# Kernel tuning notes

Hardware: AMD Instinct MI355X
Metric: run time of the kernel (lower is better)

The kernel has to match this reference:

```python
import jax, jax.numpy as jnp
import numpy as np

COORD_W, EDGE_W, COUNT_W, REG_W, CONTRA_W = 1.0, 2.0, 0.1, 0.001, 0.1
MARGIN = 1.0


def setup_inputs() -> dict:
    key = jax.random.key(0)
    ks = jax.random.split(key, 6)
    B, N, D, C = 16, 1024, 128, 2
    return {
        "predicted_coords": jax.random.normal(ks[0], (B, N, C), jnp.float32),
        "points": jax.random.normal(ks[1], (B, N, C), jnp.float32),
        "adjacency_logits": jax.random.normal(ks[2], (B, N, N), jnp.float32),
        "adjacency": jax.random.bernoulli(ks[3], 0.1, (B, N, N)).astype(jnp.float32),
        "node_masks": jnp.ones((B, N), jnp.float32),  # all nodes valid -> n_actual = N
        "predicted_count": jax.random.normal(ks[4], (B, 1), jnp.float32),
        "node_features": jax.random.normal(ks[5], (B, N, D), jnp.float32),
    }


def _bce_with_logits(logits, targets):
    # mean-reduced, numerically stable (matches F.binary_cross_entropy_with_logits)
    return jnp.mean(jnp.maximum(logits, 0.0) - logits * targets
                    + jnp.log1p(jnp.exp(-jnp.abs(logits))))


def _smooth_l1(pred, target):
    d = jnp.abs(pred - target)
    return jnp.mean(jnp.where(d < 1.0, 0.5 * d * d, d - 0.5))


def _contrastive_sample(features, adj):
    # features: [N, D], adj: [N, N]. torch.cdist pairwise euclidean via gram trick.
    nrm = jnp.sum(features * features, axis=-1)              # [N]
    sq = jnp.maximum(nrm[:, None] + nrm[None, :]
                     - 2.0 * (features @ features.T), 0.0)   # [N, N] squared dists
    n = features.shape[0]
    eye = jnp.eye(n, dtype=bool)
    pos_mask = adj > 0.5
    neg_mask = (adj <= 0.5) & (~eye)
    # positive term: mean of distances**2 over positive pairs == mean squared dist
    pos = jnp.sum(jnp.where(pos_mask, sq, 0.0)) / jnp.maximum(jnp.sum(pos_mask), 1)
    dist = jnp.sqrt(jnp.maximum(sq, 1e-12))
    hinge = jnp.square(jax.nn.relu(MARGIN - dist))
    neg = jnp.sum(jnp.where(neg_mask, hinge, 0.0)) / jnp.maximum(jnp.sum(neg_mask), 1)
    return pos + neg


def reference(predicted_coords, points, adjacency_logits, adjacency,
              node_masks, predicted_count, node_features):
    # node_masks are all ones, so the per-sample [:n_actual] slicing is the
    # full tensor; per-sample MSE/BCE means averaged over batch equal global means.
    coord_loss = jnp.mean(jnp.square(predicted_coords - points))
    edge_loss = _bce_with_logits(adjacency_logits, adjacency)
    actual_counts = jnp.sum(node_masks, axis=1)              # [B]
    count_loss = _smooth_l1(predicted_count[:, 0], actual_counts)
    reg_loss = jnp.mean(jnp.square(node_features))
    # contrastive path uses targets['adjacency'] (no predicted_adjacency key)
    contra_loss = jnp.mean(jax.vmap(_contrastive_sample)(node_features, adjacency))
    total = (COORD_W * coord_loss + EDGE_W * edge_loss + COUNT_W * count_loss
             + REG_W * reg_loss + CONTRA_W * contra_loss)
    return total, coord_loss, edge_loss, count_loss, reg_loss, contra_loss
```

## Files before the change

### kernel.cpp

```cpp
#include <hip/hip_runtime.h>
#include <hip/hip_bf16.h>

#define NN    1024
#define DD    128
#define TILE  128
#define PITCH 136
#define SQP   132

typedef __bf16 bf16_t;
typedef bf16_t bf16x8 __attribute__((ext_vector_type(8)));
typedef float  f32x4  __attribute__((ext_vector_type(4)));


__global__ __launch_bounds__(256) void small_losses(
    const float* __restrict__ pcoord, const float* __restrict__ pts,
    const float* __restrict__ masks,  const float* __restrict__ pcount,
    float* __restrict__ ws) {
  __shared__ float sh[4][2];
  float coord = 0.f, cnt = 0.f;

  const int gt = blockIdx.x * 256 + threadIdx.x;
  const int stride = 16 * 256;

  const float4* a4 = (const float4*)pcoord;
  const float4* b4 = (const float4*)pts;
  for (int i = gt; i < 8192; i += stride) {
    float4 a = a4[i], b = b4[i];
    float dx = a.x-b.x, dy = a.y-b.y, dz = a.z-b.z, dw = a.w-b.w;
    coord += dx*dx + dy*dy + dz*dz + dw*dw;
  }
  const float* m = masks + blockIdx.x * NN;
  for (int i = threadIdx.x; i < NN; i += 256) cnt += m[i];

  const int lane = threadIdx.x & 63, w = threadIdx.x >> 6;
  #pragma unroll
  for (int o = 32; o; o >>= 1) {
    coord += __shfl_xor(coord, o);
    cnt   += __shfl_xor(cnt, o);
  }
  if (lane == 0) { sh[w][0] = coord; sh[w][1] = cnt; }
  __syncthreads();
  if (threadIdx.x == 0) {
    float c = 0.f, n = 0.f;
    for (int i = 0; i < 4; ++i) { c += sh[i][0]; n += sh[i][1]; }
    atomicAdd(&ws[0], c);
    float d = fabsf(pcount[blockIdx.x] - n);
    float term = (d < 1.f) ? 0.5f * d * d : d - 0.5f;
    atomicAdd(&ws[2], term);
  }
}

__device__ __forceinline__ void loss_elem(float l, float a, float s, int grow, int gcol,
    float& bsum, float& poss, float& posc, float& negs, float& negc) {
  bsum += fmaxf(l, 0.f) - l * a + log1pf(__expf(-fabsf(l)));
  if (a > 0.5f) {
    poss += s; posc += 1.f;
  } else if (grow != gcol) {
    negc += 1.f;
    if (s < 1.f) {
      float d = sqrtf(fmaxf(s, 1e-12f));
      float h = 1.f - d;
      negs += h * h;
    }
  }
}

__global__ __launch_bounds__(256, 2) void fused_gram_bce(
    const float* __restrict__ logits, const float* __restrict__ adj,
    const float* __restrict__ feat, float* __restrict__ ws) {
  __shared__ __align__(16) char smem[2 * TILE * PITCH * sizeof(bf16_t)];
  bf16_t* lsA = (bf16_t*)smem;
  bf16_t* lsB = (bf16_t*)(smem + TILE * PITCH * sizeof(bf16_t));
  float*  sqb = (float*)smem;
  __shared__ float nrmA[TILE];
  __shared__ float nrmB[TILE];
  __shared__ float red[4][6];

  const int bx  = blockIdx.x;
  const int b   = bx >> 6;
  const int tid = bx & 63;
  const int ti  = (tid >> 3) << 7;
  const int tj  = (tid & 7)  << 7;
  const bool diag = (ti == tj);

  const int t = threadIdx.x;
  const float* fb = feat + (size_t)b * NN * DD;

  float regsum = 0.f;
  #pragma unroll
  for (int it = 0; it < 16; ++it) {
    int cid  = it * 256 + t;
    int tile = cid >> 11;
    int sub  = cid & 2047;
    int row  = sub >> 4;
    int c8   = sub & 15;
    const float* src = fb + (size_t)((tile ? tj : ti) + row) * DD + c8 * 8;
    float4 u = *(const float4*)src;
    float4 v = *(const float4*)(src + 4);
    if (diag && tile == 0)
      regsum += u.x*u.x + u.y*u.y + u.z*u.z + u.w*u.w
              + v.x*v.x + v.y*v.y + v.z*v.z + v.w*v.w;
    bf16_t* dst = (tile ? lsB : lsA) + row * PITCH + c8 * 8;
    dst[0] = (bf16_t)u.x; dst[1] = (bf16_t)u.y; dst[2] = (bf16_t)u.z; dst[3] = (bf16_t)u.w;
    dst[4] = (bf16_t)v.x; dst[5] = (bf16_t)v.y; dst[6] = (bf16_t)v.z; dst[7] = (bf16_t)v.w;
  }
  __syncthreads();

  {
    int row = t & 127;
    const bf16_t* src = (t < 128 ? lsA : lsB) + row * PITCH;
    float s = 0.f;
    #pragma unroll
    for (int c = 0; c < 16; ++c) {
      bf16x8 ch = *(const bf16x8*)(src + c * 8);
      #pragma unroll
      for (int i = 0; i < 8; ++i) { float v = (float)ch[i]; s += v * v; }
    }
    if (t < 128) nrmA[row] = s; else nrmB[row] = s;
  }
  __syncthreads();

  const int lane = t & 63;
  const int wave = t >> 6;
  const int lrow = lane & 15;
  const int quad = lane >> 4;

  f32x4 acc[2][8];
  #pragma unroll
  for (int fr = 0; fr < 2; ++fr)
    #pragma unroll
    for (int fc = 0; fc < 8; ++fc)
      acc[fr][fc] = (f32x4){0.f, 0.f, 0.f, 0.f};

  #pragma unroll
  for (int k0 = 0; k0 < DD; k0 += 32) {
    const int kc = k0 + quad * 8;
    bf16x8 aF0 = *(const bf16x8*)&lsA[(wave * 32 + 0  + lrow) * PITCH + kc];
    bf16x8 aF1 = *(const bf16x8*)&lsA[(wave * 32 + 16 + lrow) * PITCH + kc];
    bf16x8 bF[8];
    #pragma unroll
    for (int fc = 0; fc < 8; ++fc)
      bF[fc] = *(const bf16x8*)&lsB[(fc * 16 + lrow) * PITCH + kc];
    #pragma unroll
    for (int fc = 0; fc < 8; ++fc) {
      acc[0][fc] = __builtin_amdgcn_mfma_f32_16x16x32_bf16(aF0, bF[fc], acc[0][fc], 0, 0, 0);
      acc[1][fc] = __builtin_amdgcn_mfma_f32_16x16x32_bf16(aF1, bF[fc], acc[1][fc], 0, 0, 0);
    }
  }
  __syncthreads();

  #pragma unroll
  for (int fr = 0; fr < 2; ++fr) {
    const int rbase = wave * 32 + fr * 16 + quad * 4;
    #pragma unroll
    for (int fc = 0; fc < 8; ++fc) {
      const int ctile = fc * 16 + lrow;
      const float ncol = nrmB[ctile];
      #pragma unroll
      for (int r = 0; r < 4; ++r) {
        const int rtile = rbase + r;
        sqb[rtile * SQP + ctile] = fmaxf(nrmA[rtile] + ncol - 2.f * acc[fr][fc][r], 0.f);
      }
    }
  }
  __syncthreads();

  float bsum = 0.f, poss = 0.f, posc = 0.f, negs = 0.f, negc = 0.f;
  const size_t base = (size_t)b * NN * NN;
  #pragma unroll
  for (int it = 0; it < 16; ++it) {
    int cid = it * 256 + t;
    int row = cid >> 5;
    int c4  = cid & 31;
    const int grow = ti + row;
    const int gc0  = tj + c4 * 4;
    const size_t gidx = base + (size_t)grow * NN + gc0;
    float4 l = *(const float4*)(logits + gidx);
    float4 a = *(const float4*)(adj + gidx);
    float4 s = *(const float4*)&sqb[row * SQP + c4 * 4];
    loss_elem(l.x, a.x, s.x, grow, gc0 + 0, bsum, poss, posc, negs, negc);
    loss_elem(l.y, a.y, s.y, grow, gc0 + 1, bsum, poss, posc, negs, negc);
    loss_elem(l.z, a.z, s.z, grow, gc0 + 2, bsum, poss, posc, negs, negc);
    loss_elem(l.w, a.w, s.w, grow, gc0 + 3, bsum, poss, posc, negs, negc);
  }

  #pragma unroll
  for (int o = 32; o; o >>= 1) {
    bsum   += __shfl_xor(bsum, o);
    poss   += __shfl_xor(poss, o);
    posc   += __shfl_xor(posc, o);
    negs   += __shfl_xor(negs, o);
    negc   += __shfl_xor(negc, o);
    regsum += __shfl_xor(regsum, o);
  }
  if (lane == 0) {
    red[wave][0] = bsum; red[wave][1] = poss; red[wave][2] = posc;
    red[wave][3] = negs; red[wave][4] = negc; red[wave][5] = regsum;
  }
  __syncthreads();
  if (t == 0) {
    float s0 = 0.f, s1 = 0.f, s2 = 0.f, s3 = 0.f, s4 = 0.f, s5 = 0.f;
    for (int w = 0; w < 4; ++w) {
      s0 += red[w][0]; s1 += red[w][1]; s2 += red[w][2];
      s3 += red[w][3]; s4 += red[w][4]; s5 += red[w][5];
    }
    atomicAdd(&ws[3], s0);
    atomicAdd(&ws[4 + b], s1);
    atomicAdd(&ws[20 + b], s2);
    atomicAdd(&ws[36 + b], s3);
    atomicAdd(&ws[52 + b], s4);
    if (diag) atomicAdd(&ws[1], s5);
  }
}

__global__ void finalize(const float* __restrict__ ws, float* __restrict__ out) {
  if (threadIdx.x != 0 || blockIdx.x != 0) return;
  float coord = ws[0] / 32768.f;
  float reg   = ws[1] / 2097152.f;
  float cntl  = ws[2] / 16.f;
  float edge  = ws[3] / 16777216.f;
  float contra = 0.f;
  for (int b = 0; b < 16; ++b) {
    float p = ws[4 + b]  / fmaxf(ws[20 + b], 1.f);
    float n = ws[36 + b] / fmaxf(ws[52 + b], 1.f);
    contra += p + n;
  }
  contra *= (1.f / 16.f);
  float total = coord + 2.f * edge + 0.1f * cntl + 0.001f * reg + 0.1f * contra;
  out[0] = total; out[1] = coord; out[2] = edge;
  out[3] = cntl;  out[4] = reg;   out[5] = contra;
}

extern "C" void kernel_launch(void* const* d_in, const int* in_sizes, int n_in,
                              void* d_out, int out_size, void* d_ws, size_t ws_size,
                              hipStream_t stream) {
  (void)in_sizes; (void)n_in; (void)out_size; (void)ws_size;
  const float* pcoord = (const float*)d_in[0];
  const float* pts    = (const float*)d_in[1];
  const float* logits = (const float*)d_in[2];
  const float* adj    = (const float*)d_in[3];
  const float* masks  = (const float*)d_in[4];
  const float* pcount = (const float*)d_in[5];
  const float* nf     = (const float*)d_in[6];
  float* ws  = (float*)d_ws;
  float* out = (float*)d_out;

  hipMemsetAsync(ws, 0, 68 * sizeof(float), stream);
  small_losses<<<16, 256, 0, stream>>>(pcoord, pts, masks, pcount, ws);
  fused_gram_bce<<<1024, 256, 0, stream>>>(logits, adj, nf, ws);
  finalize<<<1, 64, 0, stream>>>(ws, out);
}
```

Before: 241.6 us.

## Double block size to 512 threads, split MFMA rows across 8 waves, prefetch loads

Raises the fused gram/BCE kernel to 512 threads per block with 8 waves, each computing 16 rows of the 128x128 gram tile instead of 32. This halves accumulator registers per wave and adds more waves to hide the latency of the streaming logits/adjacency reads. The BCE loop now software-prefetches the next row's float4 loads, and log1pf is replaced by the fast __logf(1+x) intrinsic. The trade-offs are that each B fragment is reloaded by more waves, and the fast log loses a little precision.

```diff
diff --git a/kernel.cpp b/kernel.cpp
--- a/kernel.cpp
+++ b/kernel.cpp
@@ -52,7 +52,7 @@
 
 __device__ __forceinline__ void loss_elem(float l, float a, float s, int grow, int gcol,
     float& bsum, float& poss, float& posc, float& negs, float& negc) {
-  bsum += fmaxf(l, 0.f) - l * a + log1pf(__expf(-fabsf(l)));
+  bsum += fmaxf(l, 0.f) - l * a + __logf(1.f + __expf(-fabsf(l)));
   if (a > 0.5f) {
     poss += s; posc += 1.f;
   } else if (grow != gcol) {
@@ -65,7 +65,7 @@
   }
 }
 
-__global__ __launch_bounds__(256, 2) void fused_gram_bce(
+__global__ __launch_bounds__(512, 4) void fused_gram_bce(
     const float* __restrict__ logits, const float* __restrict__ adj,
     const float* __restrict__ feat, float* __restrict__ ws) {
   __shared__ __align__(16) char smem[2 * TILE * PITCH * sizeof(bf16_t)];
@@ -74,7 +74,7 @@
   float*  sqb = (float*)smem;
   __shared__ float nrmA[TILE];
   __shared__ float nrmB[TILE];
-  __shared__ float red[4][6];
+  __shared__ float red[8][6];
 
   const int bx  = blockIdx.x;
   const int b   = bx >> 6;
@@ -88,8 +88,8 @@
 
   float regsum = 0.f;
   #pragma unroll
-  for (int it = 0; it < 16; ++it) {
-    int cid  = it * 256 + t;
+  for (int it = 0; it < 8; ++it) {
+    int cid  = it * 512 + t;
     int tile = cid >> 11;
     int sub  = cid & 2047;
     int row  = sub >> 4;
@@ -107,16 +107,21 @@
   __syncthreads();
 
   {
-    int row = t & 127;
-    const bf16_t* src = (t < 128 ? lsA : lsB) + row * PITCH;
+    int row  = t >> 1;
+    int half = t & 1;
+    const bf16_t* src = (row < 128 ? lsA + row * PITCH : lsB + (row - 128) * PITCH)
+                        + half * 64;
     float s = 0.f;
     #pragma unroll
-    for (int c = 0; c < 16; ++c) {
+    for (int c = 0; c < 8; ++c) {
       bf16x8 ch = *(const bf16x8*)(src + c * 8);
       #pragma unroll
       for (int i = 0; i < 8; ++i) { float v = (float)ch[i]; s += v * v; }
     }
-    if (t < 128) nrmA[row] = s; else nrmB[row] = s;
+    s += __shfl_xor(s, 1);
+    if (half == 0) {
+      if (row < 128) nrmA[row] = s; else nrmB[row - 128] = s;
+    }
   }
   __syncthreads();
 
@@ -125,33 +130,26 @@
   const int lrow = lane & 15;
   const int quad = lane >> 4;
 
-  f32x4 acc[2][8];
-  #pragma unroll
-  for (int fr = 0; fr < 2; ++fr)
-    #pragma unroll
-    for (int fc = 0; fc < 8; ++fc)
-      acc[fr][fc] = (f32x4){0.f, 0.f, 0.f, 0.f};
+  f32x4 acc[8];
+  #pragma unroll
+  for (int fc = 0; fc < 8; ++fc) acc[fc] = (f32x4){0.f, 0.f, 0.f, 0.f};
 
   #pragma unroll
   for (int k0 = 0; k0 < DD; k0 += 32) {
     const int kc = k0 + quad * 8;
-    bf16x8 aF0 = *(const bf16x8*)&lsA[(wave * 32 + 0  + lrow) * PITCH + kc];
-    bf16x8 aF1 = *(const bf16x8*)&lsA[(wave * 32 + 16 + lrow) * PITCH + kc];
+    bf16x8 aF = *(const bf16x8*)&lsA[(wave * 16 + lrow) * PITCH + kc];
     bf16x8 bF[8];
     #pragma unroll
     for (int fc = 0; fc < 8; ++fc)
       bF[fc] = *(const bf16x8*)&lsB[(fc * 16 + lrow) * PITCH + kc];
     #pragma unroll
-    for (int fc = 0; fc < 8; ++fc) {
-      acc[0][fc] = __builtin_amdgcn_mfma_f32_16x16x32_bf16(aF0, bF[fc], acc[0][fc], 0, 0, 0);
-      acc[1][fc] = __builtin_amdgcn_mfma_f32_16x16x32_bf16(aF1, bF[fc], acc[1][fc], 0, 0, 0);
-    }
-  }
-  __syncthreads();
-
-  #pragma unroll
-  for (int fr = 0; fr < 2; ++fr) {
-    const int rbase = wave * 32 + fr * 16 + quad * 4;
+    for (int fc = 0; fc < 8; ++fc)
+      acc[fc] = __builtin_amdgcn_mfma_f32_16x16x32_bf16(aF, bF[fc], acc[fc], 0, 0, 0);
+  }
+  __syncthreads();
+
+  {
+    const int rbase = wave * 16 + quad * 4;
     #pragma unroll
     for (int fc = 0; fc < 8; ++fc) {
       const int ctile = fc * 16 + lrow;
@@ -159,7 +157,7 @@
       #pragma unroll
       for (int r = 0; r < 4; ++r) {
         const int rtile = rbase + r;
-        sqb[rtile * SQP + ctile] = fmaxf(nrmA[rtile] + ncol - 2.f * acc[fr][fc][r], 0.f);
+        sqb[rtile * SQP + ctile] = fmaxf(nrmA[rtile] + ncol - 2.f * acc[fc][r], 0.f);
       }
     }
   }
@@ -167,21 +165,27 @@
 
   float bsum = 0.f, poss = 0.f, posc = 0.f, negs = 0.f, negc = 0.f;
   const size_t base = (size_t)b * NN * NN;
-  #pragma unroll
-  for (int it = 0; it < 16; ++it) {
-    int cid = it * 256 + t;
-    int row = cid >> 5;
-    int c4  = cid & 31;
+  const int c4 = t & 31, r0 = t >> 5;
+  const int gcol0 = tj + c4 * 4;
+  const float* lp = logits + base + (size_t)(ti + r0) * NN + gcol0;
+  const float* ap = adj    + base + (size_t)(ti + r0) * NN + gcol0;
+
+  float4 l0 = *(const float4*)lp;
+  float4 a0 = *(const float4*)ap;
+  #pragma unroll
+  for (int it = 0; it < 8; ++it) {
+    float4 l = l0, a = a0;
+    if (it < 7) {
+      l0 = *(const float4*)(lp + (size_t)(it + 1) * 16 * NN);
+      a0 = *(const float4*)(ap + (size_t)(it + 1) * 16 * NN);
+    }
+    const int row  = it * 16 + r0;
     const int grow = ti + row;
-    const int gc0  = tj + c4 * 4;
-    const size_t gidx = base + (size_t)grow * NN + gc0;
-    float4 l = *(const float4*)(logits + gidx);
-    float4 a = *(const float4*)(adj + gidx);
     float4 s = *(const float4*)&sqb[row * SQP + c4 * 4];
-    loss_elem(l.x, a.x, s.x, grow, gc0 + 0, bsum, poss, posc, negs, negc);
-    loss_elem(l.y, a.y, s.y, grow, gc0 + 1, bsum, poss, posc, negs, negc);
-    loss_elem(l.z, a.z, s.z, grow, gc0 + 2, bsum, poss, posc, negs, negc);
-    loss_elem(l.w, a.w, s.w, grow, gc0 + 3, bsum, poss, posc, negs, negc);
+    loss_elem(l.x, a.x, s.x, grow, gcol0 + 0, bsum, poss, posc, negs, negc);
+    loss_elem(l.y, a.y, s.y, grow, gcol0 + 1, bsum, poss, posc, negs, negc);
+    loss_elem(l.z, a.z, s.z, grow, gcol0 + 2, bsum, poss, posc, negs, negc);
+    loss_elem(l.w, a.w, s.w, grow, gcol0 + 3, bsum, poss, posc, negs, negc);
   }
 
   #pragma unroll
@@ -200,7 +204,7 @@
   __syncthreads();
   if (t == 0) {
     float s0 = 0.f, s1 = 0.f, s2 = 0.f, s3 = 0.f, s4 = 0.f, s5 = 0.f;
-    for (int w = 0; w < 4; ++w) {
+    for (int w = 0; w < 8; ++w) {
       s0 += red[w][0]; s1 += red[w][1]; s2 += red[w][2];
       s3 += red[w][3]; s4 += red[w][4]; s5 += red[w][5];
     }
@@ -247,6 +251,6 @@
 
   hipMemsetAsync(ws, 0, 68 * sizeof(float), stream);
   small_losses<<<16, 256, 0, stream>>>(pcoord, pts, masks, pcount, ws);
-  fused_gram_bce<<<1024, 256, 0, stream>>>(logits, adj, nf, ws);
+  fused_gram_bce<<<1024, 512, 0, stream>>>(logits, adj, nf, ws);
   finalize<<<1, 64, 0, stream>>>(ws, out);
 }
```

Result: faster. 200.6 us (-17.0%).
